# Kernel optimization log

Measured on AMD Instinct MI355X. Metric: run time of the kernel, lower is better.

Reference implementation:

```python
import jax, jax.numpy as jnp
import numpy as np
import math

B, S, DM = 32, 512, 1024   # batch (= groups*channels), seq_len, d_model
H, D, C = 16, 64, 8        # n_heads, d_kv, n_channels
NB, MD = 32, 128           # relative_attention_num_buckets, max_distance


def setup_inputs() -> dict:
    key = jax.random.key(0)
    ks = jax.random.split(key, 7)
    return {
        "hidden_states": jax.random.normal(ks[0], (B, S, DM), jnp.float32),
        "Wq": jax.random.normal(ks[1], (DM, H * D), jnp.float32) * 0.02,
        "Wk": jax.random.normal(ks[2], (DM, H * D), jnp.float32) * 0.02,
        "Wv": jax.random.normal(ks[3], (DM, H * D), jnp.float32) * 0.02,
        "Wo": jax.random.normal(ks[4], (H * D, DM), jnp.float32) * 0.02,
        "rel_emb": jax.random.normal(ks[5], (NB, H), jnp.float32) * 0.02,
        "beta": jax.random.normal(ks[6], (1, 1, H, 1, 1), jnp.float32) * 0.01,
    }


def _rel_bucket(relative_position, num_buckets=NB, max_distance=MD):
    # bidirectional (encoder) bucketing, faithful to T5
    nb = num_buckets // 2
    buckets = (relative_position > 0).astype(jnp.int32) * nb
    rp = jnp.abs(relative_position)
    max_exact = nb // 2
    is_small = rp < max_exact
    rp_safe = jnp.maximum(rp, 1).astype(jnp.float32)
    large = max_exact + (
        jnp.log(rp_safe / max_exact) / math.log(max_distance / max_exact) * (nb - max_exact)
    ).astype(jnp.int32)
    large = jnp.minimum(large, nb - 1)
    return buckets + jnp.where(is_small, rp, large)


def reference(hidden_states, Wq, Wk, Wv, Wo, rel_emb, beta):
    G = B // C  # groups

    def proj(W):
        # (B,S,DM) -> (B,S,H,D) -> (B,H,S,D) -> (G,C,H,S,D)
        x = (hidden_states @ W).reshape(B, S, H, D).transpose(0, 2, 1, 3)
        return x.reshape(G, C, H, S, D)

    q, k, v = proj(Wq), proj(Wk), proj(Wv)

    # relative position bias: (1,1,H,S,S)
    rel_pos = jnp.arange(S)[None, :] - jnp.arange(S)[:, None]
    bias = rel_emb[_rel_bucket(rel_pos)].transpose(2, 0, 1)[None, None]

    # local (dot-product) attention, T5-style: no 1/sqrt(d) scaling
    scores = jnp.einsum('gchsd,gchtd->gchst', q, k) + bias
    attn_w = jax.nn.softmax(scores, axis=-1)
    a_dot = jnp.einsum('gchst,gchtd->gchsd', attn_w, v)

    # compressive memory: ELU+1 feature map, summed over channels
    sk = jax.nn.elu(k) + 1.0
    M = jnp.einsum('gchsd,gchse->ghde', sk, v)   # (G,H,D,D)
    z = sk.sum(axis=3).sum(axis=1)               # (G,H,D)
    sq = jax.nn.elu(q) + 1.0
    num = jnp.einsum('gchsd,ghde->gchse', sq, M)
    den = jnp.einsum('gchsd,ghd->gchs', sq, z)[..., None] + 1e-6
    a_mem = num / den

    gate = jax.nn.sigmoid(beta)  # (1,1,H,1,1)
    out = gate * a_mem + (1.0 - gate) * a_dot

    # (G,C,H,S,D) -> (B,H,S,D) -> (B,S,H*D)
    out = out.reshape(B, H, S, D).transpose(0, 2, 1, 3).reshape(B, S, H * D)
    return out @ Wo
```

## Files before the change

kernel.cpp:

```cpp
#include <hip/hip_runtime.h>
#include <stdint.h>

typedef unsigned short u16;
typedef u16 u16x8 __attribute__((ext_vector_type(8)));
typedef u16 u16x4 __attribute__((ext_vector_type(4)));
typedef __bf16 bf16x8 __attribute__((ext_vector_type(8)));
typedef float f32x4 __attribute__((ext_vector_type(4)));

#define DEV static __device__ __forceinline__

DEV u16 f2bf(float f) {
  union { float f; uint32_t u; } v; v.f = f;
  uint32_t r = v.u + 0x7FFFu + ((v.u >> 16) & 1u);
  return (u16)(r >> 16);
}
DEV float bf2f(u16 s) {
  union { uint32_t u; float f; } v; v.u = ((uint32_t)s) << 16;
  return v.f;
}
DEV float elu1(float x) { return x > 0.f ? x + 1.f : __expf(x); }
DEV u16x8 ld8u(const u16* p) { return *reinterpret_cast<const u16x8*>(p); }

DEV f32x4 mfma16(u16x8 a, u16x8 b, f32x4 c) {
  return __builtin_amdgcn_mfma_f32_16x16x32_bf16(
      __builtin_bit_cast(bf16x8, a), __builtin_bit_cast(bf16x8, b), c, 0, 0, 0);
}
DEV void async16(void* lds, const void* g) {
  __builtin_amdgcn_global_load_lds(
      (__attribute__((address_space(1))) void*)g,
      (__attribute__((address_space(3))) void*)lds, 16, 0, 0);
}


__global__ __launch_bounds__(256) void k_cvt(const float* __restrict__ in, u16* __restrict__ out) {
  int i = blockIdx.x * 256 + threadIdx.x;
  const float4* p = reinterpret_cast<const float4*>(in) + (size_t)i * 2;
  float4 a = p[0], b = p[1];
  u16x8 o;
  o[0] = f2bf(a.x); o[1] = f2bf(a.y); o[2] = f2bf(a.z); o[3] = f2bf(a.w);
  o[4] = f2bf(b.x); o[5] = f2bf(b.y); o[6] = f2bf(b.z); o[7] = f2bf(b.w);
  reinterpret_cast<u16x8*>(out)[i] = o;
}

__global__ __launch_bounds__(1024) void k_tr(const float* __restrict__ Wq, const float* __restrict__ Wk,
                                             const float* __restrict__ Wv, const float* __restrict__ Wo,
                                             u16* __restrict__ wt, u16* __restrict__ wot) {
  __shared__ float tb[32][33];
  int mat = blockIdx.x >> 10;
  int tile = blockIdx.x & 1023;
  int n0 = (tile >> 5) * 32;
  int k0 = (tile & 31) * 32;
  const float* W = (mat == 0) ? Wq : (mat == 1) ? Wk : (mat == 2) ? Wv : Wo;
  int tx = threadIdx.x & 31, ty = threadIdx.x >> 5;
  tb[ty][tx] = W[(size_t)(k0 + ty) * 1024 + n0 + tx];
  __syncthreads();
  u16 v = f2bf(tb[tx][ty]);
  if (mat < 3) wt[(size_t)(mat * 1024 + n0 + ty) * 1024 + k0 + tx] = v;
  else         wot[(size_t)(n0 + ty) * 1024 + k0 + tx] = v;
}

__global__ void k_bias(const float* __restrict__ rel, float* __restrict__ bias) {
  int off = blockIdx.x * 256 + threadIdx.x;
  if (off >= 1023) return;
  int rp = off - 511;
  int bck = rp > 0 ? 16 : 0;
  int arp = rp < 0 ? -rp : rp;
  int idx;
  if (arp < 8) idx = arp;
  else {
    float l = logf((float)arp * 0.125f) / logf(16.0f) * 8.0f;
    int lg = 8 + (int)l;
    idx = lg < 15 ? lg : 15;
  }
  bck += idx;
  for (int h = 0; h < 16; ++h) bias[h * 1023 + off] = rel[bck * 16 + h];
}


template <int EPI, int NBN, int CPX>
__global__ __launch_bounds__(512, 2) void k_g256(const u16* __restrict__ A, const u16* __restrict__ Bt,
                                                 u16* __restrict__ oq, u16* __restrict__ ok2,
                                                 u16* __restrict__ ovt, float* __restrict__ of) {
  __shared__ __align__(16) u16 lsA[2][256 * 64];
  __shared__ __align__(16) u16 lsB[2][256 * 64];
  const int t = threadIdx.x;
  const int lane = t & 63, w = t >> 6;
  const int wm = w >> 2, wn = w & 3;
  const int lr = lane & 15, lg = lane >> 4;

  const int bid = blockIdx.x;
  const int wg = (bid & 7) * CPX + (bid >> 3);
  const int m0 = (wg / NBN) * 256;
  const int n0 = (wg % NBN) * 256;

  auto stage = [&](int kt, int slot) {
    const int k0 = kt * 64;
#pragma unroll
    for (int i = 0; i < 4; ++i) {
      int c = i * 512 + t;
      int row = c >> 3, u = c & 7;
      int us = (u ^ (row & 7)) << 3;
      async16(&lsA[slot][c * 8], A + (size_t)(m0 + row) * 1024 + k0 + us);
      async16(&lsB[slot][c * 8], Bt + (size_t)(n0 + row) * 1024 + k0 + us);
    }
  };

  f32x4 acc[8][4];
#pragma unroll
  for (int i = 0; i < 8; ++i)
#pragma unroll
    for (int j = 0; j < 4; ++j) acc[i][j] = (f32x4){0.f, 0.f, 0.f, 0.f};

  stage(0, 0);
  stage(1, 1);
  asm volatile("s_waitcnt vmcnt(8)" ::: "memory");
  __builtin_amdgcn_s_barrier();

  for (int kt = 0; kt < 16; ++kt) {
    const int slot = kt & 1;
    const u16* la = &lsA[slot][0];
    const u16* lb = &lsB[slot][0];

    u16x8 bf[4][2], af[4][2];
#pragma unroll
    for (int ni = 0; ni < 4; ++ni) {
      const int r = wn * 64 + ni * 16 + lr;
#pragma unroll
      for (int kk = 0; kk < 2; ++kk)
        bf[ni][kk] = ld8u(lb + r * 64 + (((kk * 4 + lg) ^ (r & 7)) << 3));
    }
#pragma unroll
    for (int mi = 0; mi < 4; ++mi) {
      const int r = wm * 128 + mi * 16 + lr;
#pragma unroll
      for (int kk = 0; kk < 2; ++kk)
        af[mi][kk] = ld8u(la + r * 64 + (((kk * 4 + lg) ^ (r & 7)) << 3));
    }
    __builtin_amdgcn_s_setprio(1);
#pragma unroll
    for (int mi = 0; mi < 4; ++mi)
#pragma unroll
      for (int ni = 0; ni < 4; ++ni)
#pragma unroll
        for (int kk = 0; kk < 2; ++kk)
          acc[mi][ni] = mfma16(af[mi][kk], bf[ni][kk], acc[mi][ni]);
    __builtin_amdgcn_s_setprio(0);

    u16x8 af2[4][2];
#pragma unroll
    for (int mi = 0; mi < 4; ++mi) {
      const int r = wm * 128 + 64 + mi * 16 + lr;
#pragma unroll
      for (int kk = 0; kk < 2; ++kk)
        af2[mi][kk] = ld8u(la + r * 64 + (((kk * 4 + lg) ^ (r & 7)) << 3));
    }
    asm volatile("s_waitcnt lgkmcnt(0)" ::: "memory");
    __builtin_amdgcn_s_barrier();
    if (kt + 2 < 16) stage(kt + 2, slot);

    __builtin_amdgcn_s_setprio(1);
#pragma unroll
    for (int mi = 0; mi < 4; ++mi)
#pragma unroll
      for (int ni = 0; ni < 4; ++ni)
#pragma unroll
        for (int kk = 0; kk < 2; ++kk)
          acc[4 + mi][ni] = mfma16(af2[mi][kk], bf[ni][kk], acc[4 + mi][ni]);
    __builtin_amdgcn_s_setprio(0);

    if (kt + 2 < 16) { asm volatile("s_waitcnt vmcnt(8)" ::: "memory"); }
    else             { asm volatile("s_waitcnt vmcnt(0)" ::: "memory"); }
    __builtin_amdgcn_s_barrier();
  }

  if (EPI == 0) {
    const int which = n0 >> 10;
    const int nb = (n0 & 1023) + wn * 64;
#pragma unroll
    for (int mi = 0; mi < 8; ++mi)
#pragma unroll
      for (int r = 0; r < 4; ++r) {
        int m = m0 + wm * 128 + mi * 16 + lg * 4 + r;
        int b = m >> 9, s = m & 511;
#pragma unroll
        for (int ni = 0; ni < 4; ++ni) {
          int nc = nb + ni * 16 + lr;
          int h = nc >> 6, d = nc & 63;
          int bh = b * 16 + h;
          u16 v = f2bf(acc[mi][ni][r]);
          if (which == 0)      oq[(size_t)(bh * 512 + s) * 64 + d] = v;
          else if (which == 1) ok2[(size_t)(bh * 512 + s) * 64 + d] = v;
          else                 ovt[(size_t)(bh * 64 + d) * 512 + s] = v;
        }
      }
  } else {
#pragma unroll
    for (int mi = 0; mi < 8; ++mi)
#pragma unroll
      for (int r = 0; r < 4; ++r) {
        int m = m0 + wm * 128 + mi * 16 + lg * 4 + r;
#pragma unroll
        for (int ni = 0; ni < 4; ++ni) {
          int n = n0 + wn * 64 + ni * 16 + lr;
          of[(size_t)m * 1024 + n] = acc[mi][ni][r];
        }
      }
  }
}


__global__ __launch_bounds__(256) void k_mem(const u16* __restrict__ K, const u16* __restrict__ Vt,
                                             float* __restrict__ Mp, float* __restrict__ zp) {
  __shared__ __align__(16) float sk[128 * 64];
  __shared__ __align__(16) float vv[128 * 64];
  const int bid = blockIdx.x;
  const int g = bid >> 7, h = (bid >> 3) & 15, c = bid & 7;
  const int bh = (g * 8 + c) * 16 + h;
  const u16* kp = K + (size_t)bh * 512 * 64;
  const u16* vp = Vt + (size_t)bh * 64 * 512;
  const int t = threadIdx.x;
  const int d = t & 63, eg = t >> 6;
  float acc[16];
#pragma unroll
  for (int j = 0; j < 16; ++j) acc[j] = 0.f;
  float zacc = 0.f;

  for (int s0 = 0; s0 < 512; s0 += 128) {
    __syncthreads();
    for (int j = 0; j < 32; ++j) {
      int idx = j * 256 + t;
      int ss = idx >> 6, dd = idx & 63;
      sk[idx] = elu1(bf2f(kp[(size_t)(s0 + ss) * 64 + dd]));
      int ee = idx >> 7, s2 = idx & 127;
      vv[s2 * 64 + ee] = bf2f(vp[(size_t)ee * 512 + s0 + s2]);
    }
    __syncthreads();
    for (int ss = 0; ss < 128; ++ss) {
      float a = sk[ss * 64 + d];
      if (eg == 0) zacc += a;
      const f32x4* vr = reinterpret_cast<const f32x4*>(&vv[ss * 64 + eg * 16]);
#pragma unroll
      for (int j4 = 0; j4 < 4; ++j4) {
        f32x4 vq = vr[j4];
        acc[j4 * 4 + 0] += a * vq[0];
        acc[j4 * 4 + 1] += a * vq[1];
        acc[j4 * 4 + 2] += a * vq[2];
        acc[j4 * 4 + 3] += a * vq[3];
      }
    }
  }
  float* mp = Mp + (size_t)bid * 4096 + d * 64 + eg * 16;
#pragma unroll
  for (int j = 0; j < 16; ++j) mp[j] = acc[j];
  if (eg == 0) zp[(size_t)bid * 64 + d] = zacc;
}

__global__ __launch_bounds__(256) void k_red(const float* __restrict__ Mp, const float* __restrict__ zp,
                                             u16* __restrict__ Mt, float* __restrict__ zv) {
  const int gh = blockIdx.x;
  const int t = threadIdx.x;
#pragma unroll
  for (int j = 0; j < 16; ++j) {
    int idx = j * 256 + t;
    int d = idx >> 6, e = idx & 63;
    float s = 0.f;
#pragma unroll
    for (int c = 0; c < 8; ++c) s += Mp[(size_t)(gh * 8 + c) * 4096 + idx];
    Mt[(size_t)gh * 4096 + e * 64 + d] = f2bf(s);
  }
  if (t < 64) {
    float s = 0.f;
#pragma unroll
    for (int c = 0; c < 8; ++c) s += zp[(size_t)(gh * 8 + c) * 64 + t];
    zv[gh * 64 + t] = s;
  }
}


__global__ __launch_bounds__(256, 4) void k_attn(const u16* __restrict__ Q, const u16* __restrict__ K,
                                                 const u16* __restrict__ Vt, const u16* __restrict__ Mt,
                                                 const float* __restrict__ zv, const float* __restrict__ bias,
                                                 const float* __restrict__ beta, u16* __restrict__ blend) {
  __shared__ __align__(16) u16 lK[64 * 64];
  __shared__ __align__(16) u16 lV[64 * 64];
  __shared__ __align__(16) u16 ps[4][32 * 64];
  __shared__ float lbias[1023];
  __shared__ float zs[64];
  __shared__ float rsl[4][32];
  __shared__ float dnl[4][32];

  const int bid = blockIdx.x;
  const int bh = bid >> 2, qg = bid & 3;
  const int b = bh >> 4, h = bh & 15, g = b >> 3;
  const int gh = g * 16 + h;
  const int t = threadIdx.x, lane = t & 63, w = t >> 6;
  const int lr = lane & 15, lg = lane >> 4;
  const int q0w = qg * 128 + w * 32;
  const u16* qp = Q + (size_t)bh * 512 * 64;
  const u16* kp = K + (size_t)bh * 512 * 64;
  const u16* vp = Vt + (size_t)bh * 64 * 512;
  const u16* mp = Mt + (size_t)gh * 4096;
  const float gate = 1.f / (1.f + __expf(-beta[h]));
  u16* psw = &ps[w][0];

  for (int i = t; i < 1023; i += 256) lbias[i] = bias[h * 1023 + i];
  if (t < 64) zs[t] = zv[gh * 64 + t];

  u16x8 qf[2][2];
#pragma unroll
  for (int qs = 0; qs < 2; ++qs)
#pragma unroll
    for (int dc = 0; dc < 2; ++dc)
      qf[qs][dc] = ld8u(qp + (size_t)(q0w + qs * 16 + lr) * 64 + dc * 32 + lg * 8);

#pragma unroll
  for (int i = 0; i < 2; ++i) {
    int c = w * 128 + i * 64 + lane;
    int kr = c >> 3, u = c & 7;
    async16(lK + c * 8, kp + (size_t)kr * 64 + ((u ^ (kr & 7)) << 3));
    async16(lV + c * 8, vp + (size_t)kr * 512 + ((u ^ (kr & 7)) << 3));
  }
  __syncthreads();

#pragma unroll
  for (int qs = 0; qs < 2; ++qs) {
    float sum = 0.f;
#pragma unroll
    for (int dc = 0; dc < 2; ++dc)
#pragma unroll
      for (int j = 0; j < 8; ++j)
        sum += elu1(bf2f(qf[qs][dc][j])) * zs[dc * 32 + lg * 8 + j];
    sum += __shfl_xor(sum, 16, 64);
    sum += __shfl_xor(sum, 32, 64);
    if (lane < 16) dnl[w][qs * 16 + lane] = sum + 1e-6f;
  }

  f32x4 acc[2][4];
#pragma unroll
  for (int qs = 0; qs < 2; ++qs)
#pragma unroll
    for (int es = 0; es < 4; ++es) acc[qs][es] = (f32x4){0.f, 0.f, 0.f, 0.f};
  float rs[2] = {0.f, 0.f};

  for (int kt = 0; kt < 8; ++kt) {
#pragma unroll
    for (int ks = 0; ks < 4; ++ks) {
      const int kr = ks * 16 + lr;
      u16x8 kf0 = ld8u(lK + kr * 64 + (((0 * 4 + lg) ^ (kr & 7)) << 3));
      u16x8 kf1 = ld8u(lK + kr * 64 + (((1 * 4 + lg) ^ (kr & 7)) << 3));
#pragma unroll
      for (int qs = 0; qs < 2; ++qs) {
        f32x4 s = mfma16(kf0, qf[qs][0], (f32x4){0.f, 0.f, 0.f, 0.f});
        s = mfma16(kf1, qf[qs][1], s);
        const int bbase = kt * 64 + ks * 16 + lg * 4 - (q0w + qs * 16 + lr) + 511;
        u16x4 pk;
        float lsum = 0.f;
#pragma unroll
        for (int r = 0; r < 4; ++r) {
          float p = __expf(s[r] + lbias[bbase + r]);
          lsum += p;
          pk[r] = f2bf(p);
        }
        rs[qs] += lsum;
        const int row = qs * 16 + lr;
        const int addr = row * 64 + (((ks * 2 + (lg >> 1)) ^ (row & 7)) << 3) + (lg & 1) * 4;
        *reinterpret_cast<u16x4*>(psw + addr) = pk;
      }
    }
#pragma unroll
    for (int kc = 0; kc < 2; ++kc) {
      u16x8 pf[2];
#pragma unroll
      for (int qs = 0; qs < 2; ++qs) {
        const int row = qs * 16 + lr;
        pf[qs] = ld8u(psw + row * 64 + (((kc * 4 + lg) ^ (row & 7)) << 3));
      }
#pragma unroll
      for (int es = 0; es < 4; ++es) {
        const int er = es * 16 + lr;
        u16x8 vf = ld8u(lV + er * 64 + (((kc * 4 + lg) ^ (er & 7)) << 3));
#pragma unroll
        for (int qs = 0; qs < 2; ++qs) acc[qs][es] = mfma16(pf[qs], vf, acc[qs][es]);
      }
    }
    __syncthreads();
    if (kt + 1 < 8) {
#pragma unroll
      for (int i = 0; i < 2; ++i) {
        int c = w * 128 + i * 64 + lane;
        int kr = c >> 3, u = c & 7;
        async16(lK + c * 8, kp + (size_t)((kt + 1) * 64 + kr) * 64 + ((u ^ (kr & 7)) << 3));
        async16(lV + c * 8, vp + (size_t)kr * 512 + (kt + 1) * 64 + ((u ^ (kr & 7)) << 3));
      }
    }
    __syncthreads();
  }

#pragma unroll
  for (int qs = 0; qs < 2; ++qs) {
    float v = rs[qs];
    v += __shfl_xor(v, 16, 64);
    v += __shfl_xor(v, 32, 64);
    if (lane < 16) rsl[w][qs * 16 + lane] = 1.f / v;
  }

  u16x8 sqf[2][2];
#pragma unroll
  for (int qs = 0; qs < 2; ++qs)
#pragma unroll
    for (int dc = 0; dc < 2; ++dc)
#pragma unroll
      for (int j = 0; j < 8; ++j) sqf[qs][dc][j] = f2bf(elu1(bf2f(qf[qs][dc][j])));
  f32x4 am[2][4];
#pragma unroll
  for (int qs = 0; qs < 2; ++qs)
#pragma unroll
    for (int es = 0; es < 4; ++es) am[qs][es] = (f32x4){0.f, 0.f, 0.f, 0.f};
#pragma unroll
  for (int es = 0; es < 4; ++es)
#pragma unroll
    for (int dc = 0; dc < 2; ++dc) {
      u16x8 mf = ld8u(mp + (es * 16 + lr) * 64 + dc * 32 + lg * 8);
#pragma unroll
      for (int qs = 0; qs < 2; ++qs) am[qs][es] = mfma16(sqf[qs][dc], mf, am[qs][es]);
    }

#pragma unroll
  for (int qs = 0; qs < 2; ++qs)
#pragma unroll
    for (int r = 0; r < 4; ++r) {
      const int rowl = qs * 16 + lg * 4 + r;
      const float rinv = rsl[w][rowl];
      const float den = dnl[w][rowl];
      const int q = q0w + rowl;
#pragma unroll
      for (int es = 0; es < 4; ++es) {
        float o = gate * (am[qs][es][r] / den) + (1.f - gate) * acc[qs][es][r] * rinv;
        blend[(size_t)(b * 512 + q) * 1024 + h * 64 + es * 16 + lr] = f2bf(o);
      }
    }
}


extern "C" void kernel_launch(void* const* d_in, const int* in_sizes, int n_in,
                              void* d_out, int out_size, void* d_ws, size_t ws_size,
                              hipStream_t stream) {
  (void)in_sizes; (void)n_in; (void)out_size; (void)ws_size;
  const float* hs   = (const float*)d_in[0];
  const float* Wq   = (const float*)d_in[1];
  const float* Wk   = (const float*)d_in[2];
  const float* Wv   = (const float*)d_in[3];
  const float* Wo   = (const float*)d_in[4];
  const float* rel  = (const float*)d_in[5];
  const float* beta = (const float*)d_in[6];
  float* out = (float*)d_out;

  char* ws = (char*)d_ws;
  size_t off = 0;
  auto alloc = [&](size_t bytes) -> char* {
    char* p = ws + off;
    off += (bytes + 255) & ~(size_t)255;
    return p;
  };
  u16* hsb    = (u16*)alloc(16384ull * 1024 * 2);
  u16* wt     = (u16*)alloc(3072ull * 1024 * 2);
  u16* wot    = (u16*)alloc(1024ull * 1024 * 2);
  u16* q      = (u16*)alloc(16384ull * 1024 * 2);
  u16* k      = (u16*)alloc(16384ull * 1024 * 2);
  u16* vt     = (u16*)alloc(16384ull * 1024 * 2);
  float* Mp   = (float*)alloc(512ull * 4096 * 4);
  float* zp   = (float*)alloc(512ull * 64 * 4);
  u16* Mt     = (u16*)alloc(64ull * 4096 * 2);
  float* zv   = (float*)alloc(64ull * 64 * 4);
  float* bias = (float*)alloc(16ull * 1023 * 4);
  u16* blend  = hsb;

  k_cvt<<<8192, 256, 0, stream>>>(hs, hsb);
  k_tr<<<4096, 1024, 0, stream>>>(Wq, Wk, Wv, Wo, wt, wot);
  k_bias<<<4, 256, 0, stream>>>(rel, bias);
  k_g256<0, 12, 96><<<768, 512, 0, stream>>>(hsb, wt, q, k, vt, nullptr);
  k_mem<<<512, 256, 0, stream>>>(k, vt, Mp, zp);
  k_red<<<64, 256, 0, stream>>>(Mp, zp, Mt, zv);
  k_attn<<<2048, 256, 0, stream>>>(q, k, vt, Mt, zv, bias, beta, blend);
  k_g256<1, 4, 32><<<256, 512, 0, stream>>>(blend, wot, nullptr, nullptr, nullptr, out);
}
```

Measured before the change: 401.3 us.

## Restructure GEMM main loop into 4-phase half-tile staged pipeline

Splits the GEMM K-loop into four sub-phases per K tile, each reading a half of the A or B LDS tile and issuing the next tile's global-to-LDS copies for the half that has just been consumed. The goal is finer-grained overlap between async global loads and MFMA work, with a smaller register footprint per phase. In exchange it adds more barriers and waitcnt points, and the peeled tail iterations depend on fragile vmcnt accounting.

```diff
diff --git a/kernel.cpp b/kernel.cpp
--- a/kernel.cpp
+++ b/kernel.cpp
@@ -77,6 +77,10 @@
 }
 
 
+#define BARR __builtin_amdgcn_s_barrier()
+#define LG0  asm volatile("s_waitcnt lgkmcnt(0)" ::: "memory")
+#define VMC(N) asm volatile("s_waitcnt vmcnt(" #N ")" ::: "memory")
+
 template <int EPI, int NBN, int CPX>
 __global__ __launch_bounds__(512, 2) void k_g256(const u16* __restrict__ A, const u16* __restrict__ Bt,
                                                  u16* __restrict__ oq, u16* __restrict__ ok2,
@@ -87,23 +91,31 @@
   const int lane = t & 63, w = t >> 6;
   const int wm = w >> 2, wn = w & 3;
   const int lr = lane & 15, lg = lane >> 4;
+  const int rI = t >> 3, uu = t & 7;
 
   const int bid = blockIdx.x;
   const int wg = (bid & 7) * CPX + (bid >> 3);
   const int m0 = (wg / NBN) * 256;
   const int n0 = (wg % NBN) * 256;
 
-  auto stage = [&](int kt, int slot) {
+  auto stA = [&](int kt, int slot, int half) {
     const int k0 = kt * 64;
 #pragma unroll
-    for (int i = 0; i < 4; ++i) {
-      int c = i * 512 + t;
-      int row = c >> 3, u = c & 7;
-      int us = (u ^ (row & 7)) << 3;
-      async16(&lsA[slot][c * 8], A + (size_t)(m0 + row) * 1024 + k0 + us);
-      async16(&lsB[slot][c * 8], Bt + (size_t)(n0 + row) * 1024 + k0 + us);
+    for (int i = 0; i < 2; ++i) {
+      int row = half * 64 + i * 128 + rI;
+      async16(&lsA[slot][row * 64 + uu * 8],
+              A + (size_t)(m0 + row) * 1024 + k0 + ((uu ^ (row & 7)) << 3));
     }
   };
+  auto stB = [&](int kt, int slot, int half) {
+    const int k0 = kt * 64;
+#pragma unroll
+    for (int i = 0; i < 2; ++i) {
+      int row = half * 32 + i * 128 + (rI >> 5) * 64 + (rI & 31);
+      async16(&lsB[slot][row * 64 + uu * 8],
+              Bt + (size_t)(n0 + row) * 1024 + k0 + ((uu ^ (row & 7)) << 3));
+    }
+  };
 
   f32x4 acc[8][4];
 #pragma unroll
@@ -111,66 +123,95 @@
 #pragma unroll
     for (int j = 0; j < 4; ++j) acc[i][j] = (f32x4){0.f, 0.f, 0.f, 0.f};
 
-  stage(0, 0);
-  stage(1, 1);
-  asm volatile("s_waitcnt vmcnt(8)" ::: "memory");
-  __builtin_amdgcn_s_barrier();
-
-  for (int kt = 0; kt < 16; ++kt) {
-    const int slot = kt & 1;
+#define RDA(la, grp, af)                                                      \
+  _Pragma("unroll") for (int mi = 0; mi < 4; ++mi) {                          \
+    const int r_ = wm * 128 + (grp) * 64 + mi * 16 + lr;                      \
+    _Pragma("unroll") for (int kk = 0; kk < 2; ++kk)                          \
+        af[mi][kk] = ld8u((la) + r_ * 64 + (((kk * 4 + lg) ^ (r_ & 7)) << 3));\
+  }
+#define RDB(lb, grp, bf)                                                      \
+  _Pragma("unroll") for (int ni = 0; ni < 2; ++ni) {                          \
+    const int r_ = wn * 64 + ((grp) * 2 + ni) * 16 + lr;                      \
+    _Pragma("unroll") for (int kk = 0; kk < 2; ++kk)                          \
+        bf[ni][kk] = ld8u((lb) + r_ * 64 + (((kk * 4 + lg) ^ (r_ & 7)) << 3));\
+  }
+#define MM(af, bf, MB, NB_)                                                   \
+  __builtin_amdgcn_s_setprio(1);                                              \
+  _Pragma("unroll") for (int mi = 0; mi < 4; ++mi)                            \
+  _Pragma("unroll") for (int ni = 0; ni < 2; ++ni)                            \
+  _Pragma("unroll") for (int kk = 0; kk < 2; ++kk)                            \
+      acc[(MB) + mi][(NB_) + ni] =                                            \
+          mfma16(af[mi][kk], bf[ni][kk], acc[(MB) + mi][(NB_) + ni]);         \
+  __builtin_amdgcn_s_setprio(0);
+
+  stA(0, 0, 0); stB(0, 0, 0); stB(0, 0, 1); stA(0, 0, 1); stA(1, 1, 0);
+  VMC(6);
+  BARR;
+
+  for (int T = 0; T < 14; ++T) {
+    const int slot = T & 1, os = slot ^ 1;
     const u16* la = &lsA[slot][0];
     const u16* lb = &lsB[slot][0];
-
-    u16x8 bf[4][2], af[4][2];
-#pragma unroll
-    for (int ni = 0; ni < 4; ++ni) {
-      const int r = wn * 64 + ni * 16 + lr;
-#pragma unroll
-      for (int kk = 0; kk < 2; ++kk)
-        bf[ni][kk] = ld8u(lb + r * 64 + (((kk * 4 + lg) ^ (r & 7)) << 3));
-    }
-#pragma unroll
-    for (int mi = 0; mi < 4; ++mi) {
-      const int r = wm * 128 + mi * 16 + lr;
-#pragma unroll
-      for (int kk = 0; kk < 2; ++kk)
-        af[mi][kk] = ld8u(la + r * 64 + (((kk * 4 + lg) ^ (r & 7)) << 3));
-    }
-    __builtin_amdgcn_s_setprio(1);
-#pragma unroll
-    for (int mi = 0; mi < 4; ++mi)
-#pragma unroll
-      for (int ni = 0; ni < 4; ++ni)
-#pragma unroll
-        for (int kk = 0; kk < 2; ++kk)
-          acc[mi][ni] = mfma16(af[mi][kk], bf[ni][kk], acc[mi][ni]);
-    __builtin_amdgcn_s_setprio(0);
-
-    u16x8 af2[4][2];
-#pragma unroll
-    for (int mi = 0; mi < 4; ++mi) {
-      const int r = wm * 128 + 64 + mi * 16 + lr;
-#pragma unroll
-      for (int kk = 0; kk < 2; ++kk)
-        af2[mi][kk] = ld8u(la + r * 64 + (((kk * 4 + lg) ^ (r & 7)) << 3));
-    }
-    asm volatile("s_waitcnt lgkmcnt(0)" ::: "memory");
-    __builtin_amdgcn_s_barrier();
-    if (kt + 2 < 16) stage(kt + 2, slot);
-
-    __builtin_amdgcn_s_setprio(1);
-#pragma unroll
-    for (int mi = 0; mi < 4; ++mi)
-#pragma unroll
-      for (int ni = 0; ni < 4; ++ni)
-#pragma unroll
-        for (int kk = 0; kk < 2; ++kk)
-          acc[4 + mi][ni] = mfma16(af2[mi][kk], bf[ni][kk], acc[4 + mi][ni]);
-    __builtin_amdgcn_s_setprio(0);
-
-    if (kt + 2 < 16) { asm volatile("s_waitcnt vmcnt(8)" ::: "memory"); }
-    else             { asm volatile("s_waitcnt vmcnt(0)" ::: "memory"); }
-    __builtin_amdgcn_s_barrier();
+    u16x8 a0[4][2], a1[4][2], b0[2][2], b1[2][2];
+    RDB(lb, 0, b0); RDA(la, 0, a0);
+    stB(T + 1, os, 0);
+    BARR; LG0;
+    MM(a0, b0, 0, 0);
+    VMC(6); BARR;
+    RDB(lb, 1, b1);
+    stB(T + 1, os, 1);
+    BARR; LG0;
+    MM(a0, b1, 0, 2);
+    VMC(6); BARR;
+    RDA(la, 1, a1);
+    stA(T + 1, os, 1);
+    BARR; LG0;
+    MM(a1, b0, 4, 0);
+    BARR;
+    stA(T + 2, slot, 0);
+    BARR; LG0;
+    MM(a1, b1, 4, 2);
+    VMC(6); BARR;
+  }
+  {
+    const u16* la = &lsA[0][0];
+    const u16* lb = &lsB[0][0];
+    u16x8 a0[4][2], a1[4][2], b0[2][2], b1[2][2];
+    RDB(lb, 0, b0); RDA(la, 0, a0);
+    stB(15, 1, 0);
+    BARR; LG0;
+    MM(a0, b0, 0, 0);
+    VMC(6); BARR;
+    RDB(lb, 1, b1);
+    stB(15, 1, 1);
+    BARR; LG0;
+    MM(a0, b1, 0, 2);
+    VMC(6); BARR;
+    RDA(la, 1, a1);
+    stA(15, 1, 1);
+    BARR; LG0;
+    MM(a1, b0, 4, 0);
+    BARR;
+    BARR; LG0;
+    MM(a1, b1, 4, 2);
+    VMC(4); BARR;
+  }
+  {
+    const u16* la = &lsA[1][0];
+    const u16* lb = &lsB[1][0];
+    u16x8 a0[4][2], a1[4][2], b0[2][2], b1[2][2];
+    RDB(lb, 0, b0); RDA(la, 0, a0);
+    BARR; LG0;
+    MM(a0, b0, 0, 0);
+    VMC(2); BARR;
+    RDB(lb, 1, b1);
+    BARR; LG0;
+    MM(a0, b1, 0, 2);
+    VMC(0); BARR;
+    RDA(la, 1, a1);
+    BARR; LG0;
+    MM(a1, b0, 4, 0);
+    MM(a1, b1, 4, 2);
   }
 
   if (EPI == 0) {
```

Measured after the change: 407.7 us. About the same (+1.6%).

## Rewrite compressive-memory kernel with bf16 MFMA and reorder GEMM tile mapping

Applied to the files above, without the earlier changes.

The k_mem kernel, which computes per-channel K^T V and z sums, now runs on 16x16x32 bf16 MFMA instructions instead of scalar fp32 FMAs. It stages ELU+1 of K transposed into swizzled LDS, loads V asynchronously, and reduces the per-wave partial matrices through a shared buffer. Separately, the GEMM workgroup mapping now walks M-major (m from wg % NBM) instead of N-major, which changes which tiles run concurrently and how A and B tiles are reused in L2. The MFMA path rounds the ELU features to bf16, which costs some precision, and the serial per-wave reduction adds barriers.

```diff
diff --git a/kernel.cpp b/kernel.cpp
--- a/kernel.cpp
+++ b/kernel.cpp
@@ -30,6 +30,10 @@
       (__attribute__((address_space(1))) void*)g,
       (__attribute__((address_space(3))) void*)lds, 16, 0, 0);
 }
+
+#define BARR __builtin_amdgcn_s_barrier()
+#define LG0  asm volatile("s_waitcnt lgkmcnt(0)" ::: "memory")
+#define VMC(N) asm volatile("s_waitcnt vmcnt(" #N ")" ::: "memory")
 
 
 __global__ __launch_bounds__(256) void k_cvt(const float* __restrict__ in, u16* __restrict__ out) {
@@ -77,7 +81,7 @@
 }
 
 
-template <int EPI, int NBN, int CPX>
+template <int EPI, int NBM, int CPX>
 __global__ __launch_bounds__(512, 2) void k_g256(const u16* __restrict__ A, const u16* __restrict__ Bt,
                                                  u16* __restrict__ oq, u16* __restrict__ ok2,
                                                  u16* __restrict__ ovt, float* __restrict__ of) {
@@ -90,8 +94,8 @@
 
   const int bid = blockIdx.x;
   const int wg = (bid & 7) * CPX + (bid >> 3);
-  const int m0 = (wg / NBN) * 256;
-  const int n0 = (wg % NBN) * 256;
+  const int m0 = (wg % NBM) * 256;
+  const int n0 = (wg / NBM) * 256;
 
   auto stage = [&](int kt, int slot) {
     const int k0 = kt * 64;
@@ -113,8 +117,8 @@
 
   stage(0, 0);
   stage(1, 1);
-  asm volatile("s_waitcnt vmcnt(8)" ::: "memory");
-  __builtin_amdgcn_s_barrier();
+  VMC(8);
+  BARR;
 
   for (int kt = 0; kt < 16; ++kt) {
     const int slot = kt & 1;
@@ -154,8 +158,8 @@
       for (int kk = 0; kk < 2; ++kk)
         af2[mi][kk] = ld8u(la + r * 64 + (((kk * 4 + lg) ^ (r & 7)) << 3));
     }
-    asm volatile("s_waitcnt lgkmcnt(0)" ::: "memory");
-    __builtin_amdgcn_s_barrier();
+    LG0;
+    BARR;
     if (kt + 2 < 16) stage(kt + 2, slot);
 
     __builtin_amdgcn_s_setprio(1);
@@ -168,9 +172,9 @@
           acc[4 + mi][ni] = mfma16(af2[mi][kk], bf[ni][kk], acc[4 + mi][ni]);
     __builtin_amdgcn_s_setprio(0);
 
-    if (kt + 2 < 16) { asm volatile("s_waitcnt vmcnt(8)" ::: "memory"); }
-    else             { asm volatile("s_waitcnt vmcnt(0)" ::: "memory"); }
-    __builtin_amdgcn_s_barrier();
+    if (kt + 2 < 16) { VMC(8); }
+    else             { VMC(0); }
+    BARR;
   }
 
   if (EPI == 0) {
@@ -211,48 +215,88 @@
 
 __global__ __launch_bounds__(256) void k_mem(const u16* __restrict__ K, const u16* __restrict__ Vt,
                                              float* __restrict__ Mp, float* __restrict__ zp) {
-  __shared__ __align__(16) float sk[128 * 64];
-  __shared__ __align__(16) float vv[128 * 64];
+  __shared__ __align__(16) u16 skT[64 * 128];
+  __shared__ __align__(16) u16 lV[64 * 128];
+  __shared__ float mbuf[64][65];
+  __shared__ float zsh[4][64];
   const int bid = blockIdx.x;
   const int g = bid >> 7, h = (bid >> 3) & 15, c = bid & 7;
   const int bh = (g * 8 + c) * 16 + h;
   const u16* kp = K + (size_t)bh * 512 * 64;
   const u16* vp = Vt + (size_t)bh * 64 * 512;
-  const int t = threadIdx.x;
-  const int d = t & 63, eg = t >> 6;
-  float acc[16];
-#pragma unroll
-  for (int j = 0; j < 16; ++j) acc[j] = 0.f;
+  const int t = threadIdx.x, lane = t & 63, w = t >> 6;
+  const int lr = lane & 15, lg = lane >> 4;
+  const int dmy = t & 63, sq = t >> 6;
+
+  f32x4 acc[4][4];
+#pragma unroll
+  for (int i = 0; i < 4; ++i)
+#pragma unroll
+    for (int j = 0; j < 4; ++j) acc[i][j] = (f32x4){0.f, 0.f, 0.f, 0.f};
   float zacc = 0.f;
 
   for (int s0 = 0; s0 < 512; s0 += 128) {
+#pragma unroll
+    for (int i = 0; i < 4; ++i) {
+      int c2 = i * 256 + t;
+      int row = c2 >> 4, u = c2 & 15;
+      async16(lV + c2 * 8, vp + (size_t)row * 512 + s0 + ((u ^ (row & 7)) << 3));
+    }
+#pragma unroll
+    for (int r = 0; r < 4; ++r) {
+      const int un = sq + r * 4;
+      const int ss0 = un * 8;
+      u16x8 vals;
+#pragma unroll
+      for (int j = 0; j < 8; ++j) {
+        float x = elu1(bf2f(kp[(size_t)(s0 + ss0 + j) * 64 + dmy]));
+        zacc += x;
+        vals[j] = f2bf(x);
+      }
+      *reinterpret_cast<u16x8*>(skT + dmy * 128 + ((un ^ (dmy & 7)) << 3)) = vals;
+    }
+    VMC(0);
     __syncthreads();
-    for (int j = 0; j < 32; ++j) {
-      int idx = j * 256 + t;
-      int ss = idx >> 6, dd = idx & 63;
-      sk[idx] = elu1(bf2f(kp[(size_t)(s0 + ss) * 64 + dd]));
-      int ee = idx >> 7, s2 = idx & 127;
-      vv[s2 * 64 + ee] = bf2f(vp[(size_t)ee * 512 + s0 + s2]);
-    }
+    u16x8 af[4], bfv[4];
+#pragma unroll
+    for (int ds = 0; ds < 4; ++ds) {
+      const int d = ds * 16 + lr;
+      af[ds] = ld8u(skT + d * 128 + (((w * 4 + lg) ^ (d & 7)) << 3));
+    }
+#pragma unroll
+    for (int es = 0; es < 4; ++es) {
+      const int e = es * 16 + lr;
+      bfv[es] = ld8u(lV + e * 128 + (((w * 4 + lg) ^ (e & 7)) << 3));
+    }
+#pragma unroll
+    for (int ds = 0; ds < 4; ++ds)
+#pragma unroll
+      for (int es = 0; es < 4; ++es) acc[ds][es] = mfma16(af[ds], bfv[es], acc[ds][es]);
     __syncthreads();
-    for (int ss = 0; ss < 128; ++ss) {
-      float a = sk[ss * 64 + d];
-      if (eg == 0) zacc += a;
-      const f32x4* vr = reinterpret_cast<const f32x4*>(&vv[ss * 64 + eg * 16]);
-#pragma unroll
-      for (int j4 = 0; j4 < 4; ++j4) {
-        f32x4 vq = vr[j4];
-        acc[j4 * 4 + 0] += a * vq[0];
-        acc[j4 * 4 + 1] += a * vq[1];
-        acc[j4 * 4 + 2] += a * vq[2];
-        acc[j4 * 4 + 3] += a * vq[3];
-      }
-    }
-  }
-  float* mp = Mp + (size_t)bid * 4096 + d * 64 + eg * 16;
-#pragma unroll
-  for (int j = 0; j < 16; ++j) mp[j] = acc[j];
-  if (eg == 0) zp[(size_t)bid * 64 + d] = zacc;
+  }
+
+  zsh[sq][dmy] = zacc;
+  for (int wv = 0; wv < 4; ++wv) {
+    if (w == wv) {
+#pragma unroll
+      for (int ds = 0; ds < 4; ++ds)
+#pragma unroll
+        for (int es = 0; es < 4; ++es)
+#pragma unroll
+          for (int r = 0; r < 4; ++r) {
+            int d = ds * 16 + lg * 4 + r, e = es * 16 + lr;
+            if (wv == 0) mbuf[d][e] = acc[ds][es][r];
+            else         mbuf[d][e] += acc[ds][es][r];
+          }
+    }
+    __syncthreads();
+  }
+#pragma unroll
+  for (int j = 0; j < 16; ++j) {
+    int idx = j * 256 + t;
+    Mp[(size_t)bid * 4096 + idx] = mbuf[idx >> 6][idx & 63];
+  }
+  if (t < 64) zp[(size_t)bid * 64 + t] = zsh[0][t] + zsh[1][t] + zsh[2][t] + zsh[3][t];
 }
 
 __global__ __launch_bounds__(256) void k_red(const float* __restrict__ Mp, const float* __restrict__ zp,
@@ -478,9 +522,9 @@
   k_cvt<<<8192, 256, 0, stream>>>(hs, hsb);
   k_tr<<<4096, 1024, 0, stream>>>(Wq, Wk, Wv, Wo, wt, wot);
   k_bias<<<4, 256, 0, stream>>>(rel, bias);
-  k_g256<0, 12, 96><<<768, 512, 0, stream>>>(hsb, wt, q, k, vt, nullptr);
+  k_g256<0, 64, 96><<<768, 512, 0, stream>>>(hsb, wt, q, k, vt, nullptr);
   k_mem<<<512, 256, 0, stream>>>(k, vt, Mp, zp);
   k_red<<<64, 256, 0, stream>>>(Mp, zp, Mt, zv);
   k_attn<<<2048, 256, 0, stream>>>(q, k, vt, Mt, zv, bias, beta, blend);
-  k_g256<1, 4, 32><<<256, 512, 0, stream>>>(blend, wot, nullptr, nullptr, nullptr, out);
-}
+  k_g256<1, 64, 32><<<256, 512, 0, stream>>>(blend, wot, nullptr, nullptr, nullptr, out);
+}
```

After: 379.9 us. 5.4% less time.
